# Kernel tuning notes

Measured on AMD Instinct MI355X. Metric: run time of the kernel, lower is better.

Reference implementation:

```python
import jax, jax.numpy as jnp
import numpy as np

EMBED = 1024
HEADS = 16
HEAD_DIM = EMBED // HEADS


def setup_inputs() -> dict:
    key = jax.random.key(0)
    ks = jax.random.split(key, 11)
    B, S, D = 2, 2048, EMBED
    scale = 1.0 / np.sqrt(D)
    inp = {
        "q": jax.random.normal(ks[0], (B, S, D), jnp.float32),
        "k": jax.random.normal(ks[1], (B, S, D), jnp.float32),
        "v": jax.random.normal(ks[2], (B, S, D), jnp.float32),
        "Wq": jax.random.normal(ks[3], (D, D), jnp.float32) * scale,
        "bq": jnp.zeros((D,), jnp.float32),
        "Wk": jax.random.normal(ks[4], (D, D), jnp.float32) * scale,
        "bk": jnp.zeros((D,), jnp.float32),
        "Wv": jax.random.normal(ks[5], (D, D), jnp.float32) * scale,
        "bv": jnp.zeros((D,), jnp.float32),
        "Wo": jax.random.normal(ks[6], (D, D), jnp.float32) * scale,
        "bo": jnp.zeros((D,), jnp.float32),
    }
    return inp


def _split_heads(x):
    b, n, c = x.shape
    return x.reshape(b, n, HEADS, c // HEADS).transpose(0, 2, 1, 3)  # [b,h,n,dh]


def reference(q, k, v, Wq, bq, Wk, bk, Wv, bv, Wo, bo):
    qh = _split_heads(q @ Wq + bq)
    kh = _split_heads(k @ Wk + bk)
    vh = _split_heads(v @ Wv + bv)
    scale = 1.0 / jnp.sqrt(jnp.asarray(HEAD_DIM, qh.dtype))
    att = jnp.einsum("bhqd,bhkd->bhqk", qh, kh) * scale
    att = jax.nn.softmax(att, axis=-1)
    out = jnp.einsum("bhqk,bhkd->bhqd", att, vh)
    b, h, n, dh = out.shape
    out = out.transpose(0, 2, 1, 3).reshape(b, n, h * dh)
    return out @ Wo + bo
```

## Files before the change

kernel.cpp:

```cpp
#include <hip/hip_runtime.h>
#include <hip/hip_bf16.h>
#include <stdint.h>

typedef unsigned short u16;
typedef __bf16 bf16x8 __attribute__((ext_vector_type(8)));
typedef float f32x4 __attribute__((ext_vector_type(4)));
typedef unsigned int u32x4 __attribute__((ext_vector_type(4)));
typedef unsigned int u32x2 __attribute__((ext_vector_type(2)));

#define S_LEN 2048
#define DMODEL 1024
#define NHEAD 16
#define DHEAD 64
#define MROWS 4096

__device__ __forceinline__ u16 f2b(float f) {
  __hip_bfloat16 h = __float2bfloat16(f);
  union { __hip_bfloat16 h; u16 u; } c;
  c.h = h;
  return c.u;
}
__device__ __forceinline__ unsigned int pk2(float lo, float hi) {
  return (unsigned int)f2b(lo) | ((unsigned int)f2b(hi) << 16);
}

__device__ __forceinline__ void gload16(const void* g, void* l) {
  __builtin_amdgcn_global_load_lds(
      (const __attribute__((address_space(1))) unsigned int*)(uintptr_t)g,
      (__attribute__((address_space(3))) unsigned int*)(uintptr_t)l,
      16, 0, 0);
}

__global__ __launch_bounds__(256) void prep(
    const float* __restrict__ q, const float* __restrict__ k, const float* __restrict__ v,
    const float* __restrict__ Wq, const float* __restrict__ Wk,
    const float* __restrict__ Wv, const float* __restrict__ Wo,
    u16* __restrict__ Qx, u16* __restrict__ Kx, u16* __restrict__ Vx,
    u16* __restrict__ Wqt, u16* __restrict__ Wkt,
    u16* __restrict__ Wvt, u16* __restrict__ Wot) {
  __shared__ u16 tile[64][65];
  const int z = blockIdx.z;
  const int tid = threadIdx.x;
  if (z < 3) {
    const float* src = (z == 0) ? q : (z == 1) ? k : v;
    u16* dst = (z == 0) ? Qx : (z == 1) ? Kx : Vx;
    const size_t i8 = ((size_t)blockIdx.x * 256 + tid) * 8;
    float4 a = *(const float4*)(src + i8);
    float4 b = *(const float4*)(src + i8 + 4);
    u16 o[8];
    o[0] = f2b(a.x); o[1] = f2b(a.y); o[2] = f2b(a.z); o[3] = f2b(a.w);
    o[4] = f2b(b.x); o[5] = f2b(b.y); o[6] = f2b(b.z); o[7] = f2b(b.w);
    *(u32x4*)(dst + i8) = *(const u32x4*)o;
    return;
  }
  if (blockIdx.x >= 256) return;
  const int zz = z - 3;
  const float* W = (zz == 0) ? Wq : (zz == 1) ? Wk : (zz == 2) ? Wv : Wo;
  u16* Wt = (zz == 0) ? Wqt : (zz == 1) ? Wkt : (zz == 2) ? Wvt : Wot;
  const int n0 = (blockIdx.x & 15) * 64, k0 = (blockIdx.x >> 4) * 64;
#pragma unroll
  for (int j = 0; j < 16; j++) {
    int idx = j * 256 + tid;
    int r = idx >> 6, c = idx & 63;
    tile[r][c] = f2b(W[(size_t)(k0 + r) * DMODEL + n0 + c]);
  }
  __syncthreads();
#pragma unroll
  for (int j = 0; j < 16; j++) {
    int idx = j * 256 + tid;
    int r = idx >> 6, c = idx & 63;
    Wt[(size_t)(n0 + r) * DMODEL + k0 + c] = tile[c][r];
  }
}

template <int MODE>
__device__ __forceinline__ void gemm_body(const u16* __restrict__ A,
                                          const u16* __restrict__ Bt,
                                          const float* __restrict__ bias,
                                          void* __restrict__ Cv) {
  constexpr int K = DMODEL;
  __shared__ u16 As[128 * 32];
  __shared__ u16 Bs[128 * 32];
  const int tid = threadIdx.x;
  const int wave = tid >> 6, lane = tid & 63;
  const int quad = lane >> 4, l15 = lane & 15;
  const int wr = wave >> 1, wc = wave & 1;
  const int brow = blockIdx.y, bcol = blockIdx.x;

  f32x4 acc[4][4] = {};

  for (int k0 = 0; k0 < K; k0 += 32) {
    __syncthreads();
#pragma unroll
    for (int t = 0; t < 2; t++) {
      const int slot = t * 256 + wave * 64 + lane;
      const int row = slot >> 2;
      const int col = (slot & 3) << 3;
      const int ldsb = (t * 256 + wave * 64) * 8;
      gload16(A + (size_t)(brow * 128 + row) * K + k0 + col, As + ldsb);
      gload16(Bt + (size_t)(bcol * 128 + row) * K + k0 + col, Bs + ldsb);
    }
    __syncthreads();

    bf16x8 af[4], bfm[4];
#pragma unroll
    for (int i = 0; i < 4; i++)
      af[i] = *(const bf16x8*)(As + (wr * 64 + i * 16 + l15) * 32 + quad * 8);
#pragma unroll
    for (int j = 0; j < 4; j++)
      bfm[j] = *(const bf16x8*)(Bs + (wc * 64 + j * 16 + l15) * 32 + quad * 8);
#pragma unroll
    for (int i = 0; i < 4; i++)
#pragma unroll
      for (int j = 0; j < 4; j++)
        acc[i][j] = __builtin_amdgcn_mfma_f32_16x16x32_bf16(af[i], bfm[j], acc[i][j], 0, 0, 0);
  }

#pragma unroll
  for (int i = 0; i < 4; i++)
#pragma unroll
    for (int j = 0; j < 4; j++) {
      const int col = bcol * 128 + wc * 64 + j * 16 + l15;
      const float bv = bias[col];
      if (MODE == 2) {
        const int srow = brow * 128 + wr * 64 + i * 16 + quad * 4;
        const int bb = srow >> 11, s = srow & (S_LEN - 1);
        u32x2 pd;
        pd.x = pk2(acc[i][j][0] + bv, acc[i][j][1] + bv);
        pd.y = pk2(acc[i][j][2] + bv, acc[i][j][3] + bv);
        *(u32x2*)((u16*)Cv + ((size_t)(bb * 1024 + col)) * S_LEN + s) = pd;
      } else {
#pragma unroll
        for (int r = 0; r < 4; r++) {
          const int row = brow * 128 + wr * 64 + i * 16 + quad * 4 + r;
          if (MODE == 1)
            ((float*)Cv)[(size_t)row * DMODEL + col] = acc[i][j][r] + bv;
          else
            ((u16*)Cv)[(size_t)row * DMODEL + col] = f2b(acc[i][j][r] + bv);
        }
      }
    }
}

__global__ __launch_bounds__(256) void gemm_qkv(
    const u16* __restrict__ Qx, const u16* __restrict__ Kx, const u16* __restrict__ Vx,
    const u16* __restrict__ Wqt, const u16* __restrict__ Wkt, const u16* __restrict__ Wvt,
    const float* __restrict__ bq, const float* __restrict__ bk, const float* __restrict__ bv,
    u16* __restrict__ Qp, u16* __restrict__ Kp, u16* __restrict__ Vt) {
  const int z = blockIdx.z;
  if (z == 2) {
    gemm_body<2>(Vx, Wvt, bv, Vt);
  } else {
    const u16* A = (z == 0) ? Qx : Kx;
    const u16* Bt = (z == 0) ? Wqt : Wkt;
    const float* bias = (z == 0) ? bq : bk;
    u16* C = (z == 0) ? Qp : Kp;
    gemm_body<0>(A, Bt, bias, C);
  }
}

__global__ __launch_bounds__(256) void gemm_out(
    const u16* __restrict__ A, const u16* __restrict__ Bt,
    const float* __restrict__ bias, float* __restrict__ C) {
  gemm_body<1>(A, Bt, bias, C);
}

#define EXP2SCALE 0.180336880112f
__global__ __launch_bounds__(256) void attn(const u16* __restrict__ Qp,
                                            const u16* __restrict__ Kp,
                                            const u16* __restrict__ Vt,
                                            u16* __restrict__ Op) {
  __shared__ u16 Ks[64 * 72];
  __shared__ u16 Vs[64 * 72];
  __shared__ u16 Ps[128 * 72];

  const int tid = threadIdx.x;
  const int wave = tid >> 6, lane = tid & 63;
  const int quad = lane >> 4, l15 = lane & 15;
  const int b = blockIdx.z, h = blockIdx.y, s0 = blockIdx.x * 128;

  const size_t baseK = ((size_t)(b * S_LEN)) * DMODEL + h * DHEAD;
  const size_t baseV = ((size_t)((b * NHEAD + h) * DHEAD)) * S_LEN;

  bf16x8 b1;
  {
    union { u16 a[8]; bf16x8 v; } c;
    u16 one = (l15 == 0) ? 0x3F80 : 0;
#pragma unroll
    for (int j = 0; j < 8; j++) c.a[j] = one;
    b1 = c.v;
  }

  bf16x8 qf[2][2];
#pragma unroll
  for (int rb = 0; rb < 2; rb++)
#pragma unroll
    for (int kx = 0; kx < 2; kx++)
      qf[rb][kx] = *(const bf16x8*)(Qp +
          ((size_t)(b * S_LEN + s0 + wave * 32 + rb * 16 + l15)) * DMODEL +
          h * DHEAD + kx * 32 + quad * 8);

  f32x4 oacc[2][4] = {};
  f32x4 lacc[2] = {};

  for (int kt = 0; kt < 32; kt++) {
    u32x4 kreg[2], vreg[2];
#pragma unroll
    for (int t = 0; t < 2; t++) {
      int idx = t * 256 + tid;
      int r = idx >> 3, c = (idx & 7) * 8;
      kreg[t] = *(const u32x4*)(Kp + baseK + (size_t)(kt * 64 + r) * DMODEL + c);
      vreg[t] = *(const u32x4*)(Vt + baseV + (size_t)r * S_LEN + kt * 64 + c);
    }
    __syncthreads();
#pragma unroll
    for (int t = 0; t < 2; t++) {
      int idx = t * 256 + tid;
      int r = idx >> 3, c = (idx & 7) * 8;
      *(u32x4*)(Ks + r * 72 + c) = kreg[t];
      *(u32x4*)(Vs + r * 72 + c) = vreg[t];
    }
    __syncthreads();

    f32x4 sfT[2][4] = {};
#pragma unroll
    for (int n = 0; n < 4; n++) {
#pragma unroll
      for (int kx = 0; kx < 2; kx++) {
        bf16x8 ka = *(const bf16x8*)(Ks + (n * 16 + l15) * 72 + kx * 32 + quad * 8);
        sfT[0][n] = __builtin_amdgcn_mfma_f32_16x16x32_bf16(ka, qf[0][kx], sfT[0][n], 0, 0, 0);
        sfT[1][n] = __builtin_amdgcn_mfma_f32_16x16x32_bf16(ka, qf[1][kx], sfT[1][n], 0, 0, 0);
      }
    }

#pragma unroll
    for (int rb = 0; rb < 2; rb++)
#pragma unroll
      for (int n = 0; n < 4; n++) {
        float p0 = __builtin_amdgcn_exp2f(sfT[rb][n][0] * EXP2SCALE);
        float p1 = __builtin_amdgcn_exp2f(sfT[rb][n][1] * EXP2SCALE);
        float p2 = __builtin_amdgcn_exp2f(sfT[rb][n][2] * EXP2SCALE);
        float p3 = __builtin_amdgcn_exp2f(sfT[rb][n][3] * EXP2SCALE);
        u32x2 pd;
        pd.x = pk2(p0, p1);
        pd.y = pk2(p2, p3);
        *(u32x2*)(Ps + (wave * 32 + rb * 16 + l15) * 72 + n * 16 + quad * 4) = pd;
      }

#pragma unroll
    for (int kx = 0; kx < 2; kx++) {
      bf16x8 ap0 = *(const bf16x8*)(Ps + (wave * 32 + l15) * 72 + kx * 32 + quad * 8);
      bf16x8 ap1 = *(const bf16x8*)(Ps + (wave * 32 + 16 + l15) * 72 + kx * 32 + quad * 8);
      lacc[0] = __builtin_amdgcn_mfma_f32_16x16x32_bf16(ap0, b1, lacc[0], 0, 0, 0);
      lacc[1] = __builtin_amdgcn_mfma_f32_16x16x32_bf16(ap1, b1, lacc[1], 0, 0, 0);
#pragma unroll
      for (int n = 0; n < 4; n++) {
        bf16x8 bv = *(const bf16x8*)(Vs + (n * 16 + l15) * 72 + kx * 32 + quad * 8);
        oacc[0][n] = __builtin_amdgcn_mfma_f32_16x16x32_bf16(ap0, bv, oacc[0][n], 0, 0, 0);
        oacc[1][n] = __builtin_amdgcn_mfma_f32_16x16x32_bf16(ap1, bv, oacc[1][n], 0, 0, 0);
      }
    }
  }

#pragma unroll
  for (int rb = 0; rb < 2; rb++) {
    float inv[4];
#pragma unroll
    for (int r = 0; r < 4; r++)
      inv[r] = 1.0f / __shfl(lacc[rb][r], quad * 16);
#pragma unroll
    for (int n = 0; n < 4; n++)
#pragma unroll
      for (int r = 0; r < 4; r++) {
        int row = s0 + wave * 32 + rb * 16 + quad * 4 + r;
        int col = h * DHEAD + n * 16 + l15;
        Op[((size_t)(b * S_LEN + row)) * DMODEL + col] = f2b(oacc[rb][n][r] * inv[r]);
      }
  }
}

extern "C" void kernel_launch(void* const* d_in, const int* in_sizes, int n_in,
                              void* d_out, int out_size, void* d_ws, size_t ws_size,
                              hipStream_t stream) {
  const float* q  = (const float*)d_in[0];
  const float* k  = (const float*)d_in[1];
  const float* v  = (const float*)d_in[2];
  const float* Wq = (const float*)d_in[3];
  const float* bq = (const float*)d_in[4];
  const float* Wk = (const float*)d_in[5];
  const float* bk = (const float*)d_in[6];
  const float* Wv = (const float*)d_in[7];
  const float* bv = (const float*)d_in[8];
  const float* Wo = (const float*)d_in[9];
  const float* bo = (const float*)d_in[10];

  char* w = (char*)d_ws;
  const size_t WSZ = (size_t)DMODEL * DMODEL * 2;
  const size_t XSZ = (size_t)MROWS * DMODEL * 2;
  u16* Wqt = (u16*)(w);
  u16* Wkt = (u16*)(w + WSZ);
  u16* Wvt = (u16*)(w + 2 * WSZ);
  u16* Wot = (u16*)(w + 3 * WSZ);
  u16* Qx  = (u16*)(w + 4 * WSZ);
  u16* Kx  = (u16*)(w + 4 * WSZ + XSZ);
  u16* Vx  = (u16*)(w + 4 * WSZ + 2 * XSZ);
  u16* Qp  = (u16*)(w + 4 * WSZ + 3 * XSZ);
  u16* Kp  = (u16*)(w + 4 * WSZ + 4 * XSZ);
  u16* Vt  = (u16*)(w + 4 * WSZ + 5 * XSZ);
  u16* Op  = (u16*)(w + 4 * WSZ + 6 * XSZ);

  prep<<<dim3(2048, 1, 7), 256, 0, stream>>>(q, k, v, Wq, Wk, Wv, Wo,
                                             Qx, Kx, Vx, Wqt, Wkt, Wvt, Wot);
  gemm_qkv<<<dim3(8, 32, 3), 256, 0, stream>>>(Qx, Kx, Vx, Wqt, Wkt, Wvt,
                                               bq, bk, bv, Qp, Kp, Vt);
  attn<<<dim3(16, 16, 2), 256, 0, stream>>>(Qp, Kp, Vt, Op);
  gemm_out<<<dim3(8, 32, 1), 256, 0, stream>>>(Op, Wot, bo, (float*)d_out);
}
```

Baseline: 236.0 us.

## Load K/V fragments directly to registers, swizzle attention grid, retile output GEMM

```diff
diff --git a/kernel.cpp b/kernel.cpp
--- a/kernel.cpp
+++ b/kernel.cpp
@@ -14,6 +14,11 @@
 #define DHEAD 64
 #define MROWS 4096
 
+__device__ __forceinline__ float b2f(u16 u) {
+  union { unsigned int i; float f; } c;
+  c.i = ((unsigned int)u) << 16;
+  return c.f;
+}
 __device__ __forceinline__ u16 f2b(float f) {
   __hip_bfloat16 h = __float2bfloat16(f);
   union { __hip_bfloat16 h; u16 u; } c;
@@ -133,10 +138,7 @@
 #pragma unroll
         for (int r = 0; r < 4; r++) {
           const int row = brow * 128 + wr * 64 + i * 16 + quad * 4 + r;
-          if (MODE == 1)
-            ((float*)Cv)[(size_t)row * DMODEL + col] = acc[i][j][r] + bv;
-          else
-            ((u16*)Cv)[(size_t)row * DMODEL + col] = f2b(acc[i][j][r] + bv);
+          ((u16*)Cv)[(size_t)row * DMODEL + col] = f2b(acc[i][j][r] + bv);
         }
       }
     }
@@ -162,7 +164,61 @@
 __global__ __launch_bounds__(256) void gemm_out(
     const u16* __restrict__ A, const u16* __restrict__ Bt,
     const float* __restrict__ bias, float* __restrict__ C) {
-  gemm_body<1>(A, Bt, bias, C);
+  constexpr int K = DMODEL;
+  __shared__ u16 As[64 * 32];
+  __shared__ u16 Bs[128 * 32];
+  const int tid = threadIdx.x;
+  const int wave = tid >> 6, lane = tid & 63;
+  const int quad = lane >> 4, l15 = lane & 15;
+  const int wr = wave >> 1, wc = wave & 1;
+  const int brow = blockIdx.y, bcol = blockIdx.x;
+
+  f32x4 acc[2][4] = {};
+
+  for (int k0 = 0; k0 < K; k0 += 32) {
+    __syncthreads();
+    {
+      const int slot = wave * 64 + lane;
+      const int row = slot >> 2;
+      const int col = (slot & 3) << 3;
+      gload16(A + (size_t)(brow * 64 + row) * K + k0 + col, As + wave * 512);
+    }
+#pragma unroll
+    for (int t = 0; t < 2; t++) {
+      const int slot = t * 256 + wave * 64 + lane;
+      const int row = slot >> 2;
+      const int col = (slot & 3) << 3;
+      gload16(Bt + (size_t)(bcol * 128 + row) * K + k0 + col,
+              Bs + (t * 256 + wave * 64) * 8);
+    }
+    __syncthreads();
+
+    bf16x8 af[2], bfm[4];
+#pragma unroll
+    for (int i = 0; i < 2; i++)
+      af[i] = *(const bf16x8*)(As + (wr * 32 + i * 16 + l15) * 32 + quad * 8);
+#pragma unroll
+    for (int j = 0; j < 4; j++)
+      bfm[j] = *(const bf16x8*)(Bs + (wc * 64 + j * 16 + l15) * 32 + quad * 8);
+#pragma unroll
+    for (int i = 0; i < 2; i++)
+#pragma unroll
+      for (int j = 0; j < 4; j++)
+        acc[i][j] = __builtin_amdgcn_mfma_f32_16x16x32_bf16(af[i], bfm[j], acc[i][j], 0, 0, 0);
+  }
+
+#pragma unroll
+  for (int i = 0; i < 2; i++)
+#pragma unroll
+    for (int j = 0; j < 4; j++) {
+      const int col = bcol * 128 + wc * 64 + j * 16 + l15;
+      const float bv = bias[col];
+#pragma unroll
+      for (int r = 0; r < 4; r++) {
+        const int row = brow * 64 + wr * 32 + i * 16 + quad * 4 + r;
+        C[(size_t)row * DMODEL + col] = acc[i][j][r] + bv;
+      }
+    }
 }
 
 #define EXP2SCALE 0.180336880112f
@@ -170,17 +226,18 @@
                                             const u16* __restrict__ Kp,
                                             const u16* __restrict__ Vt,
                                             u16* __restrict__ Op) {
-  __shared__ u16 Ks[64 * 72];
-  __shared__ u16 Vs[64 * 72];
   __shared__ u16 Ps[128 * 72];
 
   const int tid = threadIdx.x;
   const int wave = tid >> 6, lane = tid & 63;
   const int quad = lane >> 4, l15 = lane & 15;
-  const int b = blockIdx.z, h = blockIdx.y, s0 = blockIdx.x * 128;
-
-  const size_t baseK = ((size_t)(b * S_LEN)) * DMODEL + h * DHEAD;
-  const size_t baseV = ((size_t)((b * NHEAD + h) * DHEAD)) * S_LEN;
+  const int i = blockIdx.x;
+  const int bh = (i & 7) + 8 * (i >> 7);
+  const int qt = (i >> 3) & 15;
+  const int b = bh >> 4, h = bh & 15, s0 = qt * 128;
+
+  const u16* Kb = Kp + ((size_t)(b * S_LEN)) * DMODEL + h * DHEAD;
+  const u16* Vb = Vt + ((size_t)(b * 1024 + h * DHEAD)) * S_LEN;
 
   bf16x8 b1;
   {
@@ -195,57 +252,69 @@
 #pragma unroll
   for (int rb = 0; rb < 2; rb++)
 #pragma unroll
-    for (int kx = 0; kx < 2; kx++)
-      qf[rb][kx] = *(const bf16x8*)(Qp +
+    for (int kx = 0; kx < 2; kx++) {
+      union { u16 a[8]; bf16x8 v; u32x4 d; } c;
+      c.d = *(const u32x4*)(Qp +
           ((size_t)(b * S_LEN + s0 + wave * 32 + rb * 16 + l15)) * DMODEL +
           h * DHEAD + kx * 32 + quad * 8);
+#pragma unroll
+      for (int j = 0; j < 8; j++) c.a[j] = f2b(b2f(c.a[j]) * EXP2SCALE);
+      qf[rb][kx] = c.v;
+    }
+
+  bf16x8 kf[2][8];
+#pragma unroll
+  for (int f = 0; f < 8; f++) {
+    const int n = f >> 1, kx = f & 1;
+    kf[0][f] = *(const bf16x8*)(Kb + (size_t)(n * 16 + l15) * DMODEL + kx * 32 + quad * 8);
+  }
 
   f32x4 oacc[2][4] = {};
   f32x4 lacc[2] = {};
 
+#pragma unroll 2
   for (int kt = 0; kt < 32; kt++) {
-    u32x4 kreg[2], vreg[2];
-#pragma unroll
-    for (int t = 0; t < 2; t++) {
-      int idx = t * 256 + tid;
-      int r = idx >> 3, c = (idx & 7) * 8;
-      kreg[t] = *(const u32x4*)(Kp + baseK + (size_t)(kt * 64 + r) * DMODEL + c);
-      vreg[t] = *(const u32x4*)(Vt + baseV + (size_t)r * S_LEN + kt * 64 + c);
-    }
-    __syncthreads();
-#pragma unroll
-    for (int t = 0; t < 2; t++) {
-      int idx = t * 256 + tid;
-      int r = idx >> 3, c = (idx & 7) * 8;
-      *(u32x4*)(Ks + r * 72 + c) = kreg[t];
-      *(u32x4*)(Vs + r * 72 + c) = vreg[t];
-    }
-    __syncthreads();
+    const int cur = kt & 1, nxt = cur ^ 1;
+    __syncthreads();
+
+    bf16x8 vf[8];
+#pragma unroll
+    for (int f = 0; f < 8; f++) {
+      const int n = f >> 1, kx = f & 1;
+      vf[f] = *(const bf16x8*)(Vb +
+          (size_t)(n * 16 + l15) * S_LEN + kt * 64 + kx * 32 + quad * 8);
+    }
 
     f32x4 sfT[2][4] = {};
 #pragma unroll
-    for (int n = 0; n < 4; n++) {
+    for (int n = 0; n < 4; n++)
 #pragma unroll
       for (int kx = 0; kx < 2; kx++) {
-        bf16x8 ka = *(const bf16x8*)(Ks + (n * 16 + l15) * 72 + kx * 32 + quad * 8);
+        bf16x8 ka = kf[cur][n * 2 + kx];
         sfT[0][n] = __builtin_amdgcn_mfma_f32_16x16x32_bf16(ka, qf[0][kx], sfT[0][n], 0, 0, 0);
         sfT[1][n] = __builtin_amdgcn_mfma_f32_16x16x32_bf16(ka, qf[1][kx], sfT[1][n], 0, 0, 0);
       }
-    }
 
 #pragma unroll
     for (int rb = 0; rb < 2; rb++)
 #pragma unroll
       for (int n = 0; n < 4; n++) {
-        float p0 = __builtin_amdgcn_exp2f(sfT[rb][n][0] * EXP2SCALE);
-        float p1 = __builtin_amdgcn_exp2f(sfT[rb][n][1] * EXP2SCALE);
-        float p2 = __builtin_amdgcn_exp2f(sfT[rb][n][2] * EXP2SCALE);
-        float p3 = __builtin_amdgcn_exp2f(sfT[rb][n][3] * EXP2SCALE);
         u32x2 pd;
-        pd.x = pk2(p0, p1);
-        pd.y = pk2(p2, p3);
+        pd.x = pk2(__builtin_amdgcn_exp2f(sfT[rb][n][0]),
+                   __builtin_amdgcn_exp2f(sfT[rb][n][1]));
+        pd.y = pk2(__builtin_amdgcn_exp2f(sfT[rb][n][2]),
+                   __builtin_amdgcn_exp2f(sfT[rb][n][3]));
         *(u32x2*)(Ps + (wave * 32 + rb * 16 + l15) * 72 + n * 16 + quad * 4) = pd;
       }
+
+    if (kt < 31) {
+#pragma unroll
+      for (int f = 0; f < 8; f++) {
+        const int n = f >> 1, kx = f & 1;
+        kf[nxt][f] = *(const bf16x8*)(Kb +
+            (size_t)((kt + 1) * 64 + n * 16 + l15) * DMODEL + kx * 32 + quad * 8);
+      }
+    }
 
 #pragma unroll
     for (int kx = 0; kx < 2; kx++) {
@@ -255,9 +324,8 @@
       lacc[1] = __builtin_amdgcn_mfma_f32_16x16x32_bf16(ap1, b1, lacc[1], 0, 0, 0);
 #pragma unroll
       for (int n = 0; n < 4; n++) {
-        bf16x8 bv = *(const bf16x8*)(Vs + (n * 16 + l15) * 72 + kx * 32 + quad * 8);
-        oacc[0][n] = __builtin_amdgcn_mfma_f32_16x16x32_bf16(ap0, bv, oacc[0][n], 0, 0, 0);
-        oacc[1][n] = __builtin_amdgcn_mfma_f32_16x16x32_bf16(ap1, bv, oacc[1][n], 0, 0, 0);
+        oacc[0][n] = __builtin_amdgcn_mfma_f32_16x16x32_bf16(ap0, vf[n * 2 + kx], oacc[0][n], 0, 0, 0);
+        oacc[1][n] = __builtin_amdgcn_mfma_f32_16x16x32_bf16(ap1, vf[n * 2 + kx], oacc[1][n], 0, 0, 0);
       }
     }
   }
@@ -313,6 +381,6 @@
                                              Qx, Kx, Vx, Wqt, Wkt, Wvt, Wot);
   gemm_qkv<<<dim3(8, 32, 3), 256, 0, stream>>>(Qx, Kx, Vx, Wqt, Wkt, Wvt,
                                                bq, bk, bv, Qp, Kp, Vt);
-  attn<<<dim3(16, 16, 2), 256, 0, stream>>>(Qp, Kp, Vt, Op);
-  gemm_out<<<dim3(8, 32, 1), 256, 0, stream>>>(Op, Wot, bo, (float*)d_out);
-}
+  attn<<<dim3(512), 256, 0, stream>>>(Qp, Kp, Vt, Op);
+  gemm_out<<<dim3(8, 64), 256, 0, stream>>>(Op, Wot, bo, (float*)d_out);
+}
```

Result: slower. 291.7 us (+23.6%).
